# Optimization experiments

Measured on AMD Instinct MI355X. Metric: run time of the kernel, lower is better.

## Reference

```python
import jax, jax.numpy as jnp
import numpy as np

HEAD_DIM = 256
V_DIM = 256
HIDDEN = 1024
SCALE_BASE = 512
GAMMA = 0.96875
BATCH, SEQ = 4, 4096


def _dup_interleave(m):
    # (L, d/2) -> (L, d), duplicating each column consecutively
    return jnp.repeat(m, 2, axis=-1)


def _rotate_every_two(x):
    x1 = x[..., ::2]
    x2 = x[..., 1::2]
    return jnp.stack([-x2, x1], axis=-1).reshape(x.shape)


def _xpos(x, downscale=False):
    # x: (B, L, head_dim); offset=0 path of XPOS.forward
    B, L, Dh = x.shape
    half = Dh // 2
    scale_buf = (jnp.arange(0, Dh, 2, dtype=jnp.float32) + 0.4 * Dh) / (1.4 * Dh)  # (half,)
    pos = jnpp = jnp.arange(L, dtype=jnp.float32)
    scale = scale_buf[None, :] ** (pos / SCALE_BASE)[:, None]  # (L, half)
    inv_freq = 1.0 / (10000.0 ** (jnp.arange(half, dtype=jnp.float32) / half))
    sinusoid = pos[:, None] * inv_freq[None, :]  # (L, half)
    sin, cos = jnp.sin(sinusoid), jnp.cos(sinusoid)
    if downscale:
        scale = 1.0 / scale
    cos_s = _dup_interleave(cos * scale)  # (L, Dh)
    sin_s = _dup_interleave(sin * scale)
    return x * cos_s[None] + _rotate_every_two(x) * sin_s[None]


def _decay_matrix(L):
    n = jnp.arange(L)[:, None]
    m = jnp.arange(L)[None, :]
    mask = n >= m
    expo = jnp.where(mask, n - m, 0).astype(jnp.float32)
    return jnp.where(mask, GAMMA ** expo, 0.0)  # (L, L)


def setup_inputs() -> dict:
    key = jax.random.key(0)
    k1, k2, k3, k4 = jax.random.split(key, 4)
    X = jax.random.normal(k1, (BATCH, SEQ, HIDDEN), dtype=jnp.float32)
    W_Q = jax.random.normal(k2, (HIDDEN, HEAD_DIM), dtype=jnp.float32) / HIDDEN
    W_K = jax.random.normal(k3, (HIDDEN, HEAD_DIM), dtype=jnp.float32) / HIDDEN
    W_V = jax.random.normal(k4, (HIDDEN, V_DIM), dtype=jnp.float32) / HIDDEN
    return {"X": X, "W_Q": W_Q, "W_K": W_K, "W_V": W_V}


def reference(X, W_Q, W_K, W_V):
    L = X.shape[1]
    Q = _xpos(X @ W_Q)                      # (B, L, Dh)
    K = _xpos(X @ W_K, downscale=True)      # (B, L, Dh)
    V = X @ W_V                             # (B, L, Dv)
    D = _decay_matrix(L)                    # (L, L)
    ret = jnp.einsum('bqd,bkd->bqk', Q, K) * D[None]  # (B, L, L)
    return ret @ V                          # (B, L, Dv)
```

## Files before the change

kernel.cpp:

```cpp
#include <hip/hip_runtime.h>
#include <hip/hip_bf16.h>
#include <cstdint>
#include <cstddef>

#define L_SEQ 4096
#define BATCH_N 4
#define HID 1024
#define DH 256
#define LOG2_GAMMA (-0.045803689613124953f)
#define INV_GAMMA32 (2.7620582f)

typedef __attribute__((ext_vector_type(8))) short short8;
typedef __attribute__((ext_vector_type(4))) float floatx4;

__device__ __forceinline__ unsigned short f2bf(float f) {
    union { float f; unsigned int u; } v; v.f = f;
    unsigned int r = (v.u + 0x7FFFu + ((v.u >> 16) & 1u)) >> 16;
    return (unsigned short)r;
}

__device__ __forceinline__ void async_copy16(const unsigned short* gsrc,
                                             unsigned short* lds) {
    __builtin_amdgcn_global_load_lds(
        (const __attribute__((address_space(1))) unsigned int*)gsrc,
        (__attribute__((address_space(3))) unsigned int*)lds, 16, 0, 0);
}

__global__ __launch_bounds__(256) void prep_kernel(
    const float* __restrict__ X, unsigned short* __restrict__ Xb,
    float2* __restrict__ tabQ, float2* __restrict__ tabK,
    const float* __restrict__ WQ, const float* __restrict__ WK,
    const float* __restrict__ WV, unsigned short* __restrict__ Wt)
{
    __shared__ float Ts[64][68];
    const int bid = blockIdx.x;
    const int t   = threadIdx.x;

    if (bid < 2048) {
        const int base = bid * 256 + t;
        #pragma unroll
        for (int it = 0; it < 8; ++it) {
            const int i = (base + it * 524288) * 4;
            const float4 v = *(const float4*)&X[i];
            ushort4 p;
            p.x = f2bf(v.x); p.y = f2bf(v.y); p.z = f2bf(v.z); p.w = f2bf(v.w);
            *(ushort4*)&Xb[i] = p;
        }
    } else if (bid < 3072) {
        const int base = (bid - 2048) * 256 + t;
        #pragma unroll
        for (int e = 0; e < 2; ++e) {
            const int gid = base + e * 262144;
            const int i2  = gid >> 12;
            const int pos = gid & (L_SEQ - 1);
            const float ex  = (float)pos * (1.0f / 512.0f);
            const float sb  = ((float)(2 * i2) + 102.4f) * (1.0f / 358.4f);
            const float scQ = exp2f(log2f(sb) * ex);
            const float scK = 1.0f / scQ;
            const float invf = exp2f(-13.287712379549449f *
                                     ((float)i2 * (1.0f / 128.0f)));
            float s, c;
            sincosf((float)pos * invf, &s, &c);
            tabQ[gid] = make_float2(c * scQ, s * scQ);
            tabK[gid] = make_float2(c * scK, s * scK);
        }
    } else {
        const int idx = bid - 3072;
        const int n0 = (idx % 12) * 64;
        const int k0 = (idx / 12) * 64;
        const int seg = n0 >> 8;
        const float* __restrict__ W = (seg == 0) ? WQ : (seg == 1) ? WK : WV;
        const int nl0 = n0 & 255;

        const int r  = t >> 4;
        const int c4 = (t & 15) * 4;
        #pragma unroll
        for (int i = 0; i < 4; ++i) {
            const int kk = r + i * 16;
            const float4 v = *(const float4*)&W[(size_t)(k0 + kk) * DH + nl0 + c4];
            Ts[c4 + 0][kk] = v.x;
            Ts[c4 + 1][kk] = v.y;
            Ts[c4 + 2][kk] = v.z;
            Ts[c4 + 3][kk] = v.w;
        }
        __syncthreads();
        const int rn = t >> 3;
        const int c8 = (t & 7) * 8;
        #pragma unroll
        for (int i = 0; i < 2; ++i) {
            const int rr = rn + i * 32;
            ushort4 p0, p1;
            p0.x = f2bf(Ts[rr][c8 + 0]); p0.y = f2bf(Ts[rr][c8 + 1]);
            p0.z = f2bf(Ts[rr][c8 + 2]); p0.w = f2bf(Ts[rr][c8 + 3]);
            p1.x = f2bf(Ts[rr][c8 + 4]); p1.y = f2bf(Ts[rr][c8 + 5]);
            p1.z = f2bf(Ts[rr][c8 + 6]); p1.w = f2bf(Ts[rr][c8 + 7]);
            unsigned short* dst = &Wt[(size_t)(n0 + rr) * HID + k0 + c8];
            *(ushort4*)dst       = p0;
            *(ushort4*)(dst + 4) = p1;
        }
    }
}

__global__ __launch_bounds__(256) void gemm_qkv_kernel(
    const unsigned short* __restrict__ Wt,
    const unsigned short* __restrict__ Xb,
    const float2* __restrict__ tabQ,
    const float2* __restrict__ tabK,
    unsigned short* __restrict__ Qo,
    unsigned short* __restrict__ Ko,
    unsigned short* __restrict__ VtG)
{
    __shared__ unsigned short Wa[2][128][64];
    __shared__ unsigned short Xs[2][128][64];

    const int dblk = blockIdx.x;
    const int xcd  = dblk & 7;
    const int sq   = dblk >> 3;
    const int by   = xcd * 16 + sq / 6;
    const int bx   = sq % 6;

    const int n0 = bx * 128;
    const int p0 = by * 128;
    const int t    = threadIdx.x;
    const int w    = t >> 6;
    const int lane = t & 63;
    const int quad = lane >> 4;
    const int l16  = lane & 15;
    const int wn   = (w & 1) * 64;
    const int wp   = (w >> 1) * 64;

    floatx4 acc[4][4];
    #pragma unroll
    for (int i = 0; i < 4; ++i)
        #pragma unroll
        for (int j = 0; j < 4; ++j) acc[i][j] = (floatx4){0.f, 0.f, 0.f, 0.f};

    const int NT = HID / 64;

    const int g8 = lane >> 3;
    const int pc = lane & 7;
    const int sc = (pc ^ g8) * 8;
    auto stage = [&](int buf, int kt) {
        const int k0 = kt * 64;
        #pragma unroll
        for (int is = 0; is < 4; ++is) {
            const int gr = w * 8 + is * 32 + g8;
            const unsigned short* ga =
                &Wt[(size_t)(n0 + gr) * HID + k0 + sc];
            const unsigned short* gb =
                &Xb[(size_t)(p0 + gr) * HID + k0 + sc];
            async_copy16(ga, &Wa[buf][is * 32 + w * 8][0]);
            async_copy16(gb, &Xs[buf][is * 32 + w * 8][0]);
        }
    };

    stage(0, 0);
    stage(1, 1);

    const int xr = l16 & 7;

    for (int kt = 0; kt < NT; ++kt) {
        const int buf = kt & 1;
        if (kt + 1 < NT)
            asm volatile("s_waitcnt vmcnt(8)" ::: "memory");
        else
            asm volatile("s_waitcnt vmcnt(0)" ::: "memory");
        __builtin_amdgcn_s_barrier();

        const char* wbp = (const char*)&Wa[buf][0][0];
        const char* xbp = (const char*)&Xs[buf][0][0];
        short8 af[2][4], bfv[2][4];
        #pragma unroll
        for (int kk = 0; kk < 2; ++kk) {
            const int pk = (((kk << 2) | quad) ^ xr) << 4;
            #pragma unroll
            for (int nt = 0; nt < 4; ++nt) {
                af[kk][nt]  = *(const short8*)(wbp + (wn + nt * 16 + l16) * 128 + pk);
                bfv[kk][nt] = *(const short8*)(xbp + (wp + nt * 16 + l16) * 128 + pk);
            }
        }
        asm volatile("s_waitcnt lgkmcnt(0)" ::: "memory");
        __builtin_amdgcn_s_barrier();

        if (kt + 2 < NT) stage(buf, kt + 2);

        #pragma unroll
        for (int kk = 0; kk < 2; ++kk)
            #pragma unroll
            for (int nt = 0; nt < 4; ++nt)
                #pragma unroll
                for (int pt = 0; pt < 4; ++pt)
                    acc[nt][pt] = __builtin_amdgcn_mfma_f32_16x16x32_bf16(
                        af[kk][nt], bfv[kk][pt], acc[nt][pt], 0, 0, 0);
    }

    const int seg = n0 >> 8;
    const float2* __restrict__ tab = (seg == 1) ? tabK : tabQ;
    #pragma unroll
    for (int nt = 0; nt < 4; ++nt) {
        const int nfeat = n0 + wn + nt * 16 + quad * 4;
        const int d0 = nfeat & 255;
        #pragma unroll
        for (int pt = 0; pt < 4; ++pt) {
            const int pg  = p0 + wp + pt * 16 + l16;
            const int b   = pg >> 12;
            const int pos = pg & (L_SEQ - 1);
            if (seg == 2) {
                #pragma unroll
                for (int g = 0; g < 4; ++g)
                    VtG[(((size_t)(b * 256 + d0 + g)) << 12) + pos] =
                        f2bf(acc[nt][pt][g]);
            } else {
                float res[4];
                #pragma unroll
                for (int h = 0; h < 4; h += 2) {
                    const int i2 = (d0 + h) >> 1;
                    const float2 tc = tab[(i2 << 12) + pos];
                    const float cs = tc.x, ss = tc.y;
                    const float xe = acc[nt][pt][h], xo = acc[nt][pt][h + 1];
                    res[h]     = xe * cs - xo * ss;
                    res[h + 1] = xo * cs + xe * ss;
                }
                ushort4 pk;
                pk.x = f2bf(res[0]); pk.y = f2bf(res[1]);
                pk.z = f2bf(res[2]); pk.w = f2bf(res[3]);
                unsigned short* orow =
                    ((seg == 0) ? Qo : Ko) + (size_t)pg * DH + d0;
                *(ushort4*)orow = pk;
            }
        }
    }
}

__global__ __launch_bounds__(256) void retention_kernel(
    const unsigned short* __restrict__ Q,
    const unsigned short* __restrict__ K,
    const unsigned short* __restrict__ VtG,
    float* __restrict__ O)
{
    __shared__ unsigned short Ks[2][32][256];
    __shared__ unsigned short Vt[2][64][32];

    const int dblk = blockIdx.x;
    const int xcd  = dblk & 7;
    const int sq   = dblk >> 3;
    const int qt   = xcd * 8 + (sq & 7);
    const int b    = (sq >> 3) & 3;
    const int z    = sq >> 5;

    const int t  = threadIdx.x;
    const int q0 = qt * 64;

    const int w    = t >> 6;
    const int lane = t & 63;
    const int quad = lane >> 4;
    const int l16  = lane & 15;
    const int w16  = w * 16;

    const size_t rbase = (size_t)b * L_SEQ * DH;
    const size_t vbase = ((size_t)b * DH) << 12;

    int kst = q0 - 512; if (kst < 0) kst = 0;
    const int nsteps = ((q0 + 64) - kst) >> 5;

    const int krow = w * 2 + (lane >> 5);
    const int kscol = ((lane & 31) ^ (krow & 7)) * 8;
    const int vrow = w * 16 + (lane >> 2);
    const int vscol = ((lane & 3) ^ ((lane >> 3) & 3)) * 8;

    auto stage = [&](int buf, int k0) {
        const unsigned short* ksrc = K + rbase + (size_t)k0 * DH;
        #pragma unroll
        for (int i = 0; i < 4; ++i)
            async_copy16(&ksrc[(size_t)(i * 8 + krow) * DH + kscol],
                         &Ks[buf][i * 8 + w * 2][0]);
        async_copy16(&VtG[vbase + ((size_t)(z * 64 + vrow) << 12) + k0 + vscol],
                     &Vt[buf][w * 16][0]);
    };

    short8 qf[8];
    {
        const unsigned short* qsrc = Q + rbase + (size_t)(q0 + w16 + l16) * DH;
        #pragma unroll
        for (int dd = 0; dd < 8; ++dd)
            qf[dd] = *(const short8*)&qsrc[dd * 32 + quad * 8];
    }

    int   dint[8];
    float dec[8];
    #pragma unroll
    for (int nt = 0; nt < 2; ++nt)
        #pragma unroll
        for (int g = 0; g < 4; ++g) {
            const int idx = nt * 4 + g;
            dint[idx] = (q0 + w16 + l16) - (kst + nt * 16 + quad * 4 + g);
            dec[idx]  = exp2f((float)dint[idx] * LOG2_GAMMA);
        }

    floatx4 o[4];
    #pragma unroll
    for (int f = 0; f < 4; ++f) o[f] = (floatx4){0.f, 0.f, 0.f, 0.f};

    const int s0   = (quad & 1) * 2;
    const int idxA = (s0 * 16 + l16) * 4;
    const int idxB = idxA + 64;
    const bool lo  = (quad < 2);

    const int xk7 = l16 & 7;
    const int pvx = (quad ^ ((l16 >> 1) & 3)) << 4;

    stage(0, kst);
    asm volatile("s_waitcnt vmcnt(0)" ::: "memory");
    __builtin_amdgcn_s_barrier();

    for (int it = 0; it < nsteps; ++it) {
        const int cur = it & 1;
        const int k0  = kst + it * 32;
        if (it + 1 < nsteps) stage(cur ^ 1, k0 + 32);

        const char* kb = (const char*)&Ks[cur][0][0];
        const char* vb = (const char*)&Vt[cur][0][0];

        floatx4 sA0 = (floatx4){0.f, 0.f, 0.f, 0.f};
        floatx4 sA1 = (floatx4){0.f, 0.f, 0.f, 0.f};
        floatx4 sB0 = (floatx4){0.f, 0.f, 0.f, 0.f};
        floatx4 sB1 = (floatx4){0.f, 0.f, 0.f, 0.f};
        __builtin_amdgcn_s_setprio(1);
        #pragma unroll
        for (int dd = 0; dd < 4; ++dd) {
            const int c0 = ((dd * 4 + quad) ^ xk7) << 4;
            const int c1 = (((dd + 4) * 4 + quad) ^ xk7) << 4;
            const short8 k0f = *(const short8*)(kb + l16 * 512 + c0);
            const short8 k1f = *(const short8*)(kb + (16 + l16) * 512 + c0);
            const short8 k0g = *(const short8*)(kb + l16 * 512 + c1);
            const short8 k1g = *(const short8*)(kb + (16 + l16) * 512 + c1);
            sA0 = __builtin_amdgcn_mfma_f32_16x16x32_bf16(k0f, qf[dd], sA0, 0, 0, 0);
            sA1 = __builtin_amdgcn_mfma_f32_16x16x32_bf16(k1f, qf[dd], sA1, 0, 0, 0);
            sB0 = __builtin_amdgcn_mfma_f32_16x16x32_bf16(k0g, qf[dd + 4], sB0, 0, 0, 0);
            sB1 = __builtin_amdgcn_mfma_f32_16x16x32_bf16(k1g, qf[dd + 4], sB1, 0, 0, 0);
        }
        __builtin_amdgcn_s_setprio(0);
        const floatx4 sv0 = sA0 + sB0;
        const floatx4 sv1 = sA1 + sB1;

        unsigned int pk01[2], pk23[2];
        #pragma unroll
        for (int nt = 0; nt < 2; ++nt) {
            const floatx4 sv = nt ? sv1 : sv0;
            float pv[4];
            #pragma unroll
            for (int g = 0; g < 4; ++g) {
                const int idx = nt * 4 + g;
                pv[g] = (dint[idx] >= 0) ? sv[g] * dec[idx] : 0.0f;
            }
            pk01[nt] = ((unsigned int)f2bf(pv[1]) << 16) | (unsigned int)f2bf(pv[0]);
            pk23[nt] = ((unsigned int)f2bf(pv[3]) << 16) | (unsigned int)f2bf(pv[2]);
        }
        #pragma unroll
        for (int i = 0; i < 8; ++i) { dint[i] -= 32; dec[i] *= INV_GAMMA32; }

        const int a01_0 = __builtin_amdgcn_ds_bpermute(idxA, (int)pk01[0]);
        const int a01_1 = __builtin_amdgcn_ds_bpermute(idxA, (int)pk01[1]);
        const int a23_0 = __builtin_amdgcn_ds_bpermute(idxA, (int)pk23[0]);
        const int a23_1 = __builtin_amdgcn_ds_bpermute(idxA, (int)pk23[1]);
        const int b01_0 = __builtin_amdgcn_ds_bpermute(idxB, (int)pk01[0]);
        const int b01_1 = __builtin_amdgcn_ds_bpermute(idxB, (int)pk01[1]);
        const int b23_0 = __builtin_amdgcn_ds_bpermute(idxB, (int)pk23[0]);
        const int b23_1 = __builtin_amdgcn_ds_bpermute(idxB, (int)pk23[1]);
        union { int u[4]; short8 s8; } af;
        af.u[0] = lo ? a01_0 : a01_1;
        af.u[1] = lo ? a23_0 : a23_1;
        af.u[2] = lo ? b01_0 : b01_1;
        af.u[3] = lo ? b23_0 : b23_1;

        __builtin_amdgcn_s_setprio(1);
        #pragma unroll
        for (int f = 0; f < 4; ++f) {
            const short8 bfr =
                *(const short8*)(vb + (f * 16 + l16) * 64 + pvx);
            o[f] = __builtin_amdgcn_mfma_f32_16x16x32_bf16(af.s8, bfr, o[f], 0, 0, 0);
        }
        __builtin_amdgcn_s_setprio(0);

        asm volatile("s_waitcnt vmcnt(0)" ::: "memory");
        __builtin_amdgcn_s_barrier();
    }

    #pragma unroll
    for (int f = 0; f < 4; ++f) {
        #pragma unroll
        for (int g = 0; g < 4; ++g) {
            const int qpos = q0 + w16 + quad * 4 + g;
            O[rbase + (size_t)qpos * DH + z * 64 + f * 16 + l16] = o[f][g];
        }
    }
}

extern "C" void kernel_launch(void* const* d_in, const int* in_sizes, int n_in,
                              void* d_out, int out_size, void* d_ws, size_t ws_size,
                              hipStream_t stream)
{
    const float* X  = (const float*)d_in[0];
    const float* WQ = (const float*)d_in[1];
    const float* WK = (const float*)d_in[2];
    const float* WV = (const float*)d_in[3];
    float* out = (float*)d_out;

    const size_t per = (size_t)BATCH_N * L_SEQ * DH;
    unsigned short* Qw  = (unsigned short*)d_ws;
    unsigned short* Kw  = Qw + per;
    unsigned short* Vtw = Kw + per;
    unsigned short* Xbw = Vtw + per;
    unsigned short* Wtw = Xbw + (size_t)16384 * HID;
    float2* tabQ = (float2*)(Wtw + 786432);
    float2* tabK = tabQ + (size_t)128 * L_SEQ;

    prep_kernel<<<3264, 256, 0, stream>>>(X, Xbw, tabQ, tabK,
                                          WQ, WK, WV, Wtw);

    gemm_qkv_kernel<<<768, 256, 0, stream>>>(Wtw, Xbw, tabQ, tabK, Qw, Kw, Vtw);

    retention_kernel<<<1024, 256, 0, stream>>>(Qw, Kw, Vtw, out);
}
```

Before: 199.1 us.

## Fuse fp32-to-bf16 conversion of X into QKV GEMM staging

Removes the separate pass that converted X to a bf16 workspace copy. The QKV GEMM now loads fp32 X into registers, packs it to bf16 with v_cvt_pk_bf16_f32, and writes it to LDS, with loads issued one tile ahead. This drops a full write and re-read of the 32 MB bf16 X buffer. In exchange, each GEMM block reads fp32 X, and since six column blocks share each row tile, more raw global bytes may be read per X element. Register pressure also rises from the held float4 prefetch.

```diff
diff --git a/kernel.cpp b/kernel.cpp
--- a/kernel.cpp
+++ b/kernel.cpp
@@ -26,8 +26,13 @@
         (__attribute__((address_space(3))) unsigned int*)lds, 16, 0, 0);
 }
 
+__device__ __forceinline__ unsigned int cvt_pk_bf16(float lo, float hi) {
+    unsigned int r;
+    asm volatile("v_cvt_pk_bf16_f32 %0, %1, %2" : "=v"(r) : "v"(lo), "v"(hi));
+    return r;
+}
+
 __global__ __launch_bounds__(256) void prep_kernel(
-    const float* __restrict__ X, unsigned short* __restrict__ Xb,
     float2* __restrict__ tabQ, float2* __restrict__ tabK,
     const float* __restrict__ WQ, const float* __restrict__ WK,
     const float* __restrict__ WV, unsigned short* __restrict__ Wt)
@@ -36,18 +41,8 @@
     const int bid = blockIdx.x;
     const int t   = threadIdx.x;
 
-    if (bid < 2048) {
+    if (bid < 1024) {
         const int base = bid * 256 + t;
-        #pragma unroll
-        for (int it = 0; it < 8; ++it) {
-            const int i = (base + it * 524288) * 4;
-            const float4 v = *(const float4*)&X[i];
-            ushort4 p;
-            p.x = f2bf(v.x); p.y = f2bf(v.y); p.z = f2bf(v.z); p.w = f2bf(v.w);
-            *(ushort4*)&Xb[i] = p;
-        }
-    } else if (bid < 3072) {
-        const int base = (bid - 2048) * 256 + t;
         #pragma unroll
         for (int e = 0; e < 2; ++e) {
             const int gid = base + e * 262144;
@@ -65,7 +60,7 @@
             tabK[gid] = make_float2(c * scK, s * scK);
         }
     } else {
-        const int idx = bid - 3072;
+        const int idx = bid - 1024;
         const int n0 = (idx % 12) * 64;
         const int k0 = (idx / 12) * 64;
         const int seg = n0 >> 8;
@@ -102,8 +97,8 @@
 }
 
 __global__ __launch_bounds__(256) void gemm_qkv_kernel(
+    const float* __restrict__ X,
     const unsigned short* __restrict__ Wt,
-    const unsigned short* __restrict__ Xb,
     const float2* __restrict__ tabQ,
     const float2* __restrict__ tabK,
     unsigned short* __restrict__ Qo,
@@ -140,31 +135,59 @@
     const int g8 = lane >> 3;
     const int pc = lane & 7;
     const int sc = (pc ^ g8) * 8;
-    auto stage = [&](int buf, int kt) {
+
+    auto stageW = [&](int buf, int kt) {
         const int k0 = kt * 64;
         #pragma unroll
         for (int is = 0; is < 4; ++is) {
             const int gr = w * 8 + is * 32 + g8;
-            const unsigned short* ga =
-                &Wt[(size_t)(n0 + gr) * HID + k0 + sc];
-            const unsigned short* gb =
-                &Xb[(size_t)(p0 + gr) * HID + k0 + sc];
-            async_copy16(ga, &Wa[buf][is * 32 + w * 8][0]);
-            async_copy16(gb, &Xs[buf][is * 32 + w * 8][0]);
+            async_copy16(&Wt[(size_t)(n0 + gr) * HID + k0 + sc],
+                         &Wa[buf][is * 32 + w * 8][0]);
         }
     };
 
-    stage(0, 0);
-    stage(1, 1);
-
-    const int xr = l16 & 7;
+    float4 xr[8];
+    auto loadX = [&](int kt) {
+        const int k0 = kt * 64;
+        #pragma unroll
+        for (int is = 0; is < 4; ++is) {
+            const int gr = w * 8 + is * 32 + g8;
+            const float* xp = &X[(size_t)(p0 + gr) * HID + k0 + sc];
+            xr[is * 2]     = *(const float4*)xp;
+            xr[is * 2 + 1] = *(const float4*)(xp + 4);
+        }
+    };
+    auto writeX = [&](int buf) {
+        #pragma unroll
+        for (int is = 0; is < 4; ++is) {
+            uint4 pk;
+            pk.x = cvt_pk_bf16(xr[is * 2].x,     xr[is * 2].y);
+            pk.y = cvt_pk_bf16(xr[is * 2].z,     xr[is * 2].w);
+            pk.z = cvt_pk_bf16(xr[is * 2 + 1].x, xr[is * 2 + 1].y);
+            pk.w = cvt_pk_bf16(xr[is * 2 + 1].z, xr[is * 2 + 1].w);
+            unsigned short* dst = &Xs[buf][is * 32 + w * 8][0] + (size_t)lane * 8;
+            *(uint4*)dst = pk;
+        }
+    };
+
+    loadX(0);
+    stageW(0, 0);
+    writeX(0);
+    loadX(1);
+    stageW(1, 1);
+    writeX(1);
+    if (NT > 2) loadX(2);
+
+    const int xr7 = l16 & 7;
 
     for (int kt = 0; kt < NT; ++kt) {
         const int buf = kt & 1;
-        if (kt + 1 < NT)
-            asm volatile("s_waitcnt vmcnt(8)" ::: "memory");
+        if (kt + 2 < NT)
+            asm volatile("s_waitcnt vmcnt(12) lgkmcnt(0)" ::: "memory");
+        else if (kt + 1 < NT)
+            asm volatile("s_waitcnt vmcnt(4) lgkmcnt(0)" ::: "memory");
         else
-            asm volatile("s_waitcnt vmcnt(0)" ::: "memory");
+            asm volatile("s_waitcnt vmcnt(0) lgkmcnt(0)" ::: "memory");
         __builtin_amdgcn_s_barrier();
 
         const char* wbp = (const char*)&Wa[buf][0][0];
@@ -172,7 +195,7 @@
         short8 af[2][4], bfv[2][4];
         #pragma unroll
         for (int kk = 0; kk < 2; ++kk) {
-            const int pk = (((kk << 2) | quad) ^ xr) << 4;
+            const int pk = (((kk << 2) | quad) ^ xr7) << 4;
             #pragma unroll
             for (int nt = 0; nt < 4; ++nt) {
                 af[kk][nt]  = *(const short8*)(wbp + (wn + nt * 16 + l16) * 128 + pk);
@@ -182,7 +205,11 @@
         asm volatile("s_waitcnt lgkmcnt(0)" ::: "memory");
         __builtin_amdgcn_s_barrier();
 
-        if (kt + 2 < NT) stage(buf, kt + 2);
+        if (kt + 2 < NT) {
+            writeX(buf);
+            stageW(buf, kt + 2);
+            if (kt + 3 < NT) loadX(kt + 3);
+        }
 
         #pragma unroll
         for (int kk = 0; kk < 2; ++kk)
@@ -410,15 +437,13 @@
     unsigned short* Qw  = (unsigned short*)d_ws;
     unsigned short* Kw  = Qw + per;
     unsigned short* Vtw = Kw + per;
-    unsigned short* Xbw = Vtw + per;
-    unsigned short* Wtw = Xbw + (size_t)16384 * HID;
+    unsigned short* Wtw = Vtw + per;
     float2* tabQ = (float2*)(Wtw + 786432);
     float2* tabK = tabQ + (size_t)128 * L_SEQ;
 
-    prep_kernel<<<3264, 256, 0, stream>>>(X, Xbw, tabQ, tabK,
-                                          WQ, WK, WV, Wtw);
-
-    gemm_qkv_kernel<<<768, 256, 0, stream>>>(Wtw, Xbw, tabQ, tabK, Qw, Kw, Vtw);
+    prep_kernel<<<1216, 256, 0, stream>>>(tabQ, tabK, WQ, WK, WV, Wtw);
+
+    gemm_qkv_kernel<<<768, 256, 0, stream>>>(X, Wtw, tabQ, tabK, Qw, Kw, Vtw);
 
     retention_kernel<<<1024, 256, 0, stream>>>(Qw, Kw, Vtw, out);
 }
```

After: 196.9 us. No clear change (-1.1%).
